# Kernel optimization log

Measured on AMD Instinct MI355X. Metric: run time of the kernel, lower is better.

Reference implementation:

```python
import math
import jax, jax.numpy as jnp
import numpy as np
from jax.scipy.special import xlogy, gammaln

HEADS = 8
DIM_KEY = 64
NUM_REL_POS_FEATURES = 192


def get_positional_embed(n, feature_size):
    # distances: [-n+1, ..., n-1], length 2n-1
    dist = jnp.arange(-n + 1, n)
    adist = jnp.abs(dist).astype(jnp.float32)[:, None]  # (2n-1, 1)
    num_basis = feature_size // 6  # 3 feature fns * 2 (sign-augmented)
    seq_len = n
    # exponential half-life features
    max_range = math.log(seq_len) / math.log(2.0)
    half_life = 2.0 ** jnp.linspace(3.0, max_range, num_basis)  # min_half_life=3.0
    feat_exp = jnp.exp(-math.log(2.0) / half_life[None, :] * adist)
    # central mask features
    center_widths = 2.0 ** jnp.arange(1, num_basis + 1) - 1.0
    feat_cm = (center_widths[None, :] > adist).astype(jnp.float32)
    # gamma pdf features
    stddev = seq_len / (2 * num_basis)
    start_mean = seq_len / num_basis
    mean = jnp.linspace(start_mean, float(seq_len), num_basis)[None, :]
    concentration = (mean / stddev) ** 2
    rate = mean / (stddev ** 2)
    log_unnorm = xlogy(concentration - 1.0, adist) - rate * adist
    log_norm = gammaln(concentration) - concentration * jnp.log(rate)
    prob = jnp.exp(log_unnorm - log_norm) + 1e-8
    feat_gamma = prob / jnp.max(prob, axis=-1, keepdims=True)
    emb = jnp.concatenate([feat_exp, feat_cm, feat_gamma], axis=-1)  # (2n-1, fs/2)
    sign = jnp.sign(dist).astype(jnp.float32)[:, None]
    return jnp.concatenate([emb, sign * emb], axis=-1)  # (2n-1, fs)


def relative_shift(x):
    # x: (b, h, n, 2n-1) -> (b, h, n, n) Transformer-XL shift
    b, h, t1, t2 = x.shape
    x = jnp.pad(x, ((0, 0), (0, 0), (0, 0), (1, 0)))  # (b,h,t1,t2+1)
    x = x.reshape(b, h, t2 + 1, t1)[:, :, 1:, :].reshape(b, h, t1, t2)
    return x[..., : (t2 + 2) // 2]


def setup_inputs() -> dict:
    key = jax.random.key(0)
    ks = jax.random.split(key, 8)
    dim = 1536
    b, n = 2, 1536
    hdk = HEADS * DIM_KEY  # 512
    hdv = HEADS * 192      # 1536
    s = 0.02
    return {
        'x': jax.random.normal(ks[0], (b, n, dim), jnp.float32),
        'Wq': jax.random.normal(ks[1], (hdk, dim), jnp.float32) * s,
        'Wk': jax.random.normal(ks[2], (hdk, dim), jnp.float32) * s,
        'Wv': jax.random.normal(ks[3], (hdv, dim), jnp.float32) * s,
        'Wrel': jax.random.normal(ks[4], (hdk, NUM_REL_POS_FEATURES), jnp.float32) * s,
        'Wout': jax.random.normal(ks[5], (dim, hdv), jnp.float32) * s,
        'b_out': jnp.zeros((dim,), jnp.float32),
        'rel_content_bias': jax.random.normal(ks[6], (1, HEADS, 1, DIM_KEY), jnp.float32),
        'rel_pos_bias': jax.random.normal(ks[7], (1, HEADS, 1, DIM_KEY), jnp.float32),
    }


def reference(x, Wq, Wk, Wv, Wrel, Wout, b_out, rel_content_bias, rel_pos_bias):
    b, n, dim = x.shape
    h = HEADS
    scale = DIM_KEY ** -0.5

    def split_heads(t):  # (b, n, h*d) -> (b, h, n, d)
        return t.reshape(b, n, h, -1).transpose(0, 2, 1, 3)

    q = split_heads(jnp.einsum('bnd,fd->bnf', x, Wq)) * scale
    k = split_heads(jnp.einsum('bnd,fd->bnf', x, Wk))
    v = split_heads(jnp.einsum('bnd,fd->bnf', x, Wv))

    content_logits = jnp.einsum('bhid,bhjd->bhij', q + rel_content_bias, k)

    positions = get_positional_embed(n, NUM_REL_POS_FEATURES)  # (2n-1, fs)
    rel_k = jnp.einsum('jf,ef->je', positions, Wrel).reshape(2 * n - 1, h, DIM_KEY)
    rel_k = rel_k.transpose(1, 0, 2)  # (h, 2n-1, dk)
    rel_logits = jnp.einsum('bhid,hjd->bhij', q + rel_pos_bias, rel_k)
    rel_logits = relative_shift(rel_logits)  # (b, h, n, n)

    attn = jax.nn.softmax(content_logits + rel_logits, axis=-1)
    out = jnp.einsum('bhij,bhjd->bhid', attn, v)
    out = out.transpose(0, 2, 1, 3).reshape(b, n, -1)  # (b, n, h*dv)
    return jnp.einsum('bnf,df->bnd', out, Wout) + b_out
```

## Files before the change

kernel.cpp:

```cpp
#include <hip/hip_runtime.h>
#include <cmath>

typedef unsigned short u16;
typedef unsigned int u32;
typedef short frag8 __attribute__((ext_vector_type(8)));
typedef float f32x4 __attribute__((ext_vector_type(4)));

#define DEVINL __device__ __forceinline__

DEVINL float bf2f(u16 v) { return __uint_as_float(((u32)v) << 16); }
DEVINL u16 f2bf(float f) {
    u32 u = __float_as_uint(f);
    u32 r = (u + 0x7fffu + ((u >> 16) & 1u)) >> 16;
    return (u16)r;
}
DEVINL u32 pack2(float a, float b) { return (u32)f2bf(a) | ((u32)f2bf(b) << 16); }
DEVINL void async_copy16(const u16* g, u16* l) {
    __builtin_amdgcn_global_load_lds((const __attribute__((address_space(1))) u32*)g,
                                     (__attribute__((address_space(3))) u32*)l, 16, 0, 0);
}
DEVINL f32x4 mfma_bf16(frag8 a, frag8 b, f32x4 c) {
    return __builtin_amdgcn_mfma_f32_16x16x32_bf16(a, b, c, 0, 0, 0);
}

__global__ __launch_bounds__(256) void convert_kernel(
        const float* __restrict__ s0, const float* __restrict__ s1,
        const float* __restrict__ s2, const float* __restrict__ s3,
        const float* __restrict__ s4, u16* __restrict__ dst) {
    const int c0 = 589824, c1 = 98304, c2 = 98304, c3 = 294912;
    const int total = 1376256;
    for (int c = blockIdx.x * blockDim.x + threadIdx.x; c < total;
         c += gridDim.x * blockDim.x) {
        const float* src; int off;
        if (c < c0) { src = s0; off = c; }
        else if (c < c0 + c1) { src = s1; off = c - c0; }
        else if (c < c0 + c1 + c2) { src = s2; off = c - c0 - c1; }
        else if (c < c0 + c1 + c2 + c3) { src = s3; off = c - c0 - c1 - c2; }
        else { src = s4; off = c - c0 - c1 - c2 - c3; }
        float4 a = ((const float4*)src)[off * 2];
        float4 b = ((const float4*)src)[off * 2 + 1];
        uint4 o;
        o.x = pack2(a.x, a.y); o.y = pack2(a.z, a.w);
        o.z = pack2(b.x, b.y); o.w = pack2(b.z, b.w);
        ((uint4*)dst)[c] = o;
    }
}

DEVINL double lgamma_stirling(double z) {
    double zi = 1.0 / z, zi2 = zi * zi;
    return (z - 0.5) * log(z) - z + 0.91893853320467274178
         + zi * (1.0 / 12.0) - zi * zi2 * (1.0 / 360.0) + zi * zi2 * zi2 * (1.0 / 1260.0);
}

__global__ __launch_bounds__(256) void embed_relk_kernel(const float* __restrict__ Wrel,
                                                         u16* __restrict__ relk) {
    __shared__ float pos[16][192];
    __shared__ float inv_hl[32], cwid[32], cm1[32], rateS[32];
    __shared__ double lognS[32];
    __shared__ float gmax[16];
    int t = threadIdx.x;
    int u0b = blockIdx.x * 16;

    if (t < 32) {
        double step = (10.584962500721156 - 3.0) / 31.0;
        double hl = exp2(3.0 + t * step);
        inv_hl[t] = (float)(1.0 / hl);
        cwid[t] = exp2f((float)(t + 1)) - 1.0f;
        double mean = 48.0 * (t + 1);
        double conc = (mean / 24.0) * (mean / 24.0);
        double rate = mean / 576.0;
        cm1[t] = (float)(conc - 1.0);
        rateS[t] = (float)rate;
        lognS[t] = lgamma_stirling(conc) - conc * log(rate);
    }
    __syncthreads();

    for (int idx = t; idx < 512; idx += 256) {
        int ul = idx >> 5, bs = idx & 31;
        int dist = u0b + ul - 1535;
        float ad = fabsf((float)dist);
        pos[ul][bs] = exp2f(-ad * inv_hl[bs]);
        pos[ul][32 + bs] = (cwid[bs] > ad) ? 1.0f : 0.0f;
        double prob = 0.0;
        if (dist != 0) {
            double adD = (double)ad;
            prob = exp((double)cm1[bs] * log(adD) - (double)rateS[bs] * adD - lognS[bs]);
        }
        pos[ul][64 + bs] = (float)(prob + 1e-8);
    }
    __syncthreads();
    if (t < 16) {
        float g = 0.f;
        #pragma unroll
        for (int bsx = 0; bsx < 32; bsx++) g = fmaxf(g, pos[t][64 + bsx]);
        gmax[t] = g;
    }
    __syncthreads();
    for (int idx = t; idx < 16 * 96; idx += 256) {
        int ul = idx / 96, f = idx - ul * 96;
        float v = pos[ul][f];
        if (f >= 64) { v = v / gmax[ul]; pos[ul][f] = v; }
        int dist = u0b + ul - 1535;
        float sg = (dist > 0) ? 1.f : ((dist < 0) ? -1.f : 0.f);
        pos[ul][96 + f] = sg * v;
    }
    __syncthreads();

    int e0 = t * 2;
    const float* w0 = Wrel + e0 * 192;
    const float* w1 = w0 + 192;
    float a0[16], a1[16];
    #pragma unroll
    for (int ul = 0; ul < 16; ul++) { a0[ul] = 0.f; a1[ul] = 0.f; }
    for (int f = 0; f < 192; f++) {
        float wa = w0[f], wb = w1[f];
        #pragma unroll
        for (int ul = 0; ul < 16; ul++) {
            float p = pos[ul][f];
            a0[ul] = fmaf(p, wa, a0[ul]);
            a1[ul] = fmaf(p, wb, a1[ul]);
        }
    }
    int h0 = e0 >> 6, d0 = e0 & 63;
    int h1 = (e0 + 1) >> 6, d1 = (e0 + 1) & 63;
    for (int ul = 0; ul < 16; ul++) {
        int u = u0b + ul;
        relk[(h0 * 3072 + u) * 64 + d0] = f2bf(a0[ul]);
        relk[(h1 * 3072 + u) * 64 + d1] = f2bf(a1[ul]);
    }
}

DEVINL void gemm128_mainloop(const u16* __restrict__ A, const u16* __restrict__ B,
                             int K, f32x4 acc[4][4], u16* As, u16* Bs) {
    int tid = threadIdx.x;
    int lane = tid & 63, wave = tid >> 6;
    int wm = (wave >> 1) * 64, wn = (wave & 1) * 64;
    int fm = lane & 15, fq = lane >> 4;
    for (int k0 = 0; k0 < K; k0 += 32) {
        #pragma unroll
        for (int p = 0; p < 2; p++) {
            int e = (p * 256 + tid) * 8;
            int r = e >> 5, c = e & 31;
            async_copy16(A + r * K + k0 + c, As + e);
            async_copy16(B + r * K + k0 + c, Bs + e);
        }
        __syncthreads();
        frag8 af[4], bfr[4];
        #pragma unroll
        for (int mi = 0; mi < 4; mi++) af[mi] = *(const frag8*)&As[(wm + 16 * mi + fm) * 32 + fq * 8];
        #pragma unroll
        for (int ni = 0; ni < 4; ni++) bfr[ni] = *(const frag8*)&Bs[(wn + 16 * ni + fm) * 32 + fq * 8];
        #pragma unroll
        for (int mi = 0; mi < 4; mi++)
            #pragma unroll
            for (int ni = 0; ni < 4; ni++)
                acc[mi][ni] = mfma_bf16(af[mi], bfr[ni], acc[mi][ni]);
        __syncthreads();
    }
}

__global__ __launch_bounds__(256) void gemm_qkv_kernel(
        const u16* __restrict__ X, const u16* __restrict__ Wq, const u16* __restrict__ Wk,
        const u16* __restrict__ Wv, const float* __restrict__ cbias, const float* __restrict__ pbias,
        u16* __restrict__ qc, u16* __restrict__ qp, u16* __restrict__ kws, u16* __restrict__ vt) {
    __shared__ __align__(16) u16 As[128 * 32];
    __shared__ __align__(16) u16 Bs[128 * 32];
    int m0 = blockIdx.x * 128, n0 = blockIdx.y * 128;
    const u16* Bp; int brow;
    if (n0 < 512)       { Bp = Wq; brow = n0; }
    else if (n0 < 1024) { Bp = Wk; brow = n0 - 512; }
    else                { Bp = Wv; brow = n0 - 1024; }
    f32x4 acc[4][4];
    #pragma unroll
    for (int i = 0; i < 4; i++)
        #pragma unroll
        for (int j = 0; j < 4; j++) acc[i][j] = (f32x4){0.f, 0.f, 0.f, 0.f};
    gemm128_mainloop(X + m0 * 1536, Bp + brow * 1536, 1536, acc, As, Bs);

    int tid = threadIdx.x, lane = tid & 63, wave = tid >> 6;
    int wm = (wave >> 1) * 64, wn = (wave & 1) * 64, fm = lane & 15, fq = lane >> 4;
    #pragma unroll
    for (int mi = 0; mi < 4; mi++) {
        #pragma unroll
        for (int ni = 0; ni < 4; ni++) {
            int col = n0 + wn + 16 * ni + fm;
            int rbase = m0 + wm + 16 * mi + fq * 4;
            #pragma unroll
            for (int reg = 0; reg < 4; reg++) {
                int row = rbase + reg;
                float v = acc[mi][ni][reg];
                int b = row >= 1536 ? 1 : 0;
                int i = row - b * 1536;
                if (n0 < 512) {
                    float qv = v * 0.125f;
                    int idx = ((b * 8 + (col >> 6)) * 1536 + i) * 64 + (col & 63);
                    qc[idx] = f2bf(qv + cbias[col]);
                    qp[idx] = f2bf(qv + pbias[col]);
                } else if (n0 < 1024) {
                    int c2 = col - 512;
                    kws[((b * 8 + (c2 >> 6)) * 1536 + i) * 64 + (c2 & 63)] = f2bf(v);
                } else {
                    int c2 = col - 1024;
                    int hh = c2 / 192, dd = c2 - hh * 192;
                    vt[((b * 8 + hh) * 192 + dd) * 1536 + i] = f2bf(v);
                }
            }
        }
    }
}

__global__ __launch_bounds__(256) void attn_kernel(
        const u16* __restrict__ qc, const u16* __restrict__ qp, const u16* __restrict__ kws,
        const u16* __restrict__ vt, const u16* __restrict__ relk, u16* __restrict__ ao) {
    __shared__ __align__(16) u16 k_lds[64 * 64];
    __shared__ __align__(16) u16 vt_lds[192 * 64];
    __shared__ __align__(16) u16 relk_lds[96 * 64];
    __shared__ __align__(16) float S_lds[32 * 64];
    __shared__ __align__(16) u16 P_lds[32 * 64];
    __shared__ float mstate[32], lstate[32], alpha_lds[32];
    float* R_lds = (float*)relk_lds;

    const int n = 1536;
    int bh = blockIdx.y, b = bh >> 3, h = bh & 7;
    int i0 = blockIdx.x * 32;
    const u16* qcP = qc + bh * n * 64;
    const u16* qpP = qp + bh * n * 64;
    const u16* kP  = kws + bh * n * 64;
    const u16* vtP = vt + bh * 192 * n;
    const u16* rkP = relk + h * 3072 * 64;

    int tid = threadIdx.x, lane = tid & 63, w = tid >> 6, fm = lane & 15, fq = lane >> 4;
    if (tid < 32) { mstate[tid] = __int_as_float(0xff800000); lstate[tid] = 0.f; }

    frag8 aqc[2][2], aqp[2][2];
    #pragma unroll
    for (int mi = 0; mi < 2; mi++)
        #pragma unroll
        for (int ks = 0; ks < 2; ks++) {
            int off = (i0 + 16 * mi + fm) * 64 + ks * 32 + fq * 8;
            aqc[mi][ks] = *(const frag8*)(qcP + off);
            aqp[mi][ks] = *(const frag8*)(qpP + off);
        }

    f32x4 acc_o[2][3];
    #pragma unroll
    for (int mi = 0; mi < 2; mi++)
        #pragma unroll
        for (int dj = 0; dj < 3; dj++) acc_o[mi][dj] = (f32x4){0.f, 0.f, 0.f, 0.f};

    for (int jt = 0; jt < 24; jt++) {
        int j0 = jt * 64;
        __syncthreads();
        #pragma unroll
        for (int p = 0; p < 2; p++) {
            int e = (p * 256 + tid) * 8;
            async_copy16(kP + (j0 + (e >> 6)) * 64 + (e & 63), k_lds + e);
        }
        #pragma unroll
        for (int p = 0; p < 6; p++) {
            int e = (p * 256 + tid) * 8;
            async_copy16(vtP + (e >> 6) * n + j0 + (e & 63), vt_lds + e);
        }
        int u0 = n - 1 + j0 - i0 - 31;
        #pragma unroll
        for (int p = 0; p < 3; p++) {
            int e = (p * 256 + tid) * 8;
            async_copy16(rkP + (u0 + (e >> 6)) * 64 + (e & 63), relk_lds + e);
        }
        __syncthreads();

        f32x4 acc_s[2];
        acc_s[0] = (f32x4){0.f, 0.f, 0.f, 0.f};
        acc_s[1] = (f32x4){0.f, 0.f, 0.f, 0.f};
        #pragma unroll
        for (int ks = 0; ks < 2; ks++) {
            frag8 bk = *(const frag8*)&k_lds[(16 * w + fm) * 64 + ks * 32 + fq * 8];
            acc_s[0] = mfma_bf16(aqc[0][ks], bk, acc_s[0]);
            acc_s[1] = mfma_bf16(aqc[1][ks], bk, acc_s[1]);
        }
        f32x4 acc_r[3];
        int uis[3], rmis[3];
        #pragma unroll
        for (int tt = 0; tt < 3; tt++) {
            int tv = w + tt * 4;
            int rmi = (tv >= 6) ? 1 : 0;
            int ui = tv - rmi * 6;
            uis[tt] = ui; rmis[tt] = rmi;
            acc_r[tt] = (f32x4){0.f, 0.f, 0.f, 0.f};
            #pragma unroll
            for (int ks = 0; ks < 2; ks++) {
                frag8 br = *(const frag8*)&relk_lds[(16 * ui + fm) * 64 + ks * 32 + fq * 8];
                acc_r[tt] = mfma_bf16(aqp[rmi][ks], br, acc_r[tt]);
            }
        }
        __syncthreads();

        #pragma unroll
        for (int mi = 0; mi < 2; mi++)
            #pragma unroll
            for (int reg = 0; reg < 4; reg++)
                S_lds[(16 * mi + fq * 4 + reg) * 64 + 16 * w + fm] = acc_s[mi][reg];
        #pragma unroll
        for (int tt = 0; tt < 3; tt++)
            #pragma unroll
            for (int reg = 0; reg < 4; reg++)
                R_lds[(16 * rmis[tt] + fq * 4 + reg) * 96 + 16 * uis[tt] + fm] = acc_r[tt][reg];
        __syncthreads();

        int li = tid >> 3, c0 = (tid & 7) * 8;
        float sv[8];
        float mx = __int_as_float(0xff800000);
        #pragma unroll
        for (int e = 0; e < 8; e++) {
            int c = c0 + e;
            sv[e] = S_lds[li * 64 + c] + R_lds[li * 96 + c - li + 31];
            mx = fmaxf(mx, sv[e]);
        }
        mx = fmaxf(mx, __shfl_xor(mx, 1));
        mx = fmaxf(mx, __shfl_xor(mx, 2));
        mx = fmaxf(mx, __shfl_xor(mx, 4));
        float mo = mstate[li];
        float mn = fmaxf(mo, mx);
        float al = __expf(mo - mn);
        float sum = 0.f;
        #pragma unroll
        for (int e = 0; e < 8; e++) {
            float pv = __expf(sv[e] - mn);
            sum += pv;
            P_lds[li * 64 + c0 + e] = f2bf(pv);
        }
        sum += __shfl_xor(sum, 1);
        sum += __shfl_xor(sum, 2);
        sum += __shfl_xor(sum, 4);
        if ((tid & 7) == 0) {
            mstate[li] = mn;
            lstate[li] = lstate[li] * al + sum;
            alpha_lds[li] = al;
        }
        __syncthreads();

        #pragma unroll
        for (int mi = 0; mi < 2; mi++)
            #pragma unroll
            for (int reg = 0; reg < 4; reg++) {
                float al2 = alpha_lds[16 * mi + fq * 4 + reg];
                #pragma unroll
                for (int dj = 0; dj < 3; dj++) acc_o[mi][dj][reg] *= al2;
            }
        frag8 ap[2][2];
        #pragma unroll
        for (int mi = 0; mi < 2; mi++)
            #pragma unroll
            for (int ks = 0; ks < 2; ks++)
                ap[mi][ks] = *(const frag8*)&P_lds[(16 * mi + fm) * 64 + ks * 32 + fq * 8];
        #pragma unroll
        for (int dj = 0; dj < 3; dj++) {
            #pragma unroll
            for (int ks = 0; ks < 2; ks++) {
                frag8 bv = *(const frag8*)&vt_lds[(16 * (3 * w + dj) + fm) * 64 + ks * 32 + fq * 8];
                acc_o[0][dj] = mfma_bf16(ap[0][ks], bv, acc_o[0][dj]);
                acc_o[1][dj] = mfma_bf16(ap[1][ks], bv, acc_o[1][dj]);
            }
        }
    }

    #pragma unroll
    for (int mi = 0; mi < 2; mi++)
        #pragma unroll
        for (int dj = 0; dj < 3; dj++)
            #pragma unroll
            for (int reg = 0; reg < 4; reg++) {
                int rl = 16 * mi + fq * 4 + reg;
                float lsum = lstate[rl];
                int row = b * 1536 + i0 + rl;
                int col = h * 192 + 16 * (3 * w + dj) + fm;
                ao[row * 1536 + col] = f2bf(acc_o[mi][dj][reg] / lsum);
            }
}

__global__ __launch_bounds__(256) void gemm_out_kernel(
        const u16* __restrict__ A, const u16* __restrict__ W, const float* __restrict__ bias,
        float* __restrict__ out) {
    __shared__ __align__(16) u16 As[128 * 32];
    __shared__ __align__(16) u16 Bs[128 * 32];
    int m0 = blockIdx.x * 128, n0 = blockIdx.y * 128;
    f32x4 acc[4][4];
    #pragma unroll
    for (int i = 0; i < 4; i++)
        #pragma unroll
        for (int j = 0; j < 4; j++) acc[i][j] = (f32x4){0.f, 0.f, 0.f, 0.f};
    gemm128_mainloop(A + m0 * 1536, W + n0 * 1536, 1536, acc, As, Bs);

    int tid = threadIdx.x, lane = tid & 63, wave = tid >> 6;
    int wm = (wave >> 1) * 64, wn = (wave & 1) * 64, fm = lane & 15, fq = lane >> 4;
    #pragma unroll
    for (int mi = 0; mi < 4; mi++) {
        #pragma unroll
        for (int ni = 0; ni < 4; ni++) {
            int col = n0 + wn + 16 * ni + fm;
            int rbase = m0 + wm + 16 * mi + fq * 4;
            float bv = bias[col];
            #pragma unroll
            for (int reg = 0; reg < 4; reg++) {
                int row = rbase + reg;
                out[row * 1536 + col] = acc[mi][ni][reg] + bv;
            }
        }
    }
}

extern "C" void kernel_launch(void* const* d_in, const int* in_sizes, int n_in,
                              void* d_out, int out_size, void* d_ws, size_t ws_size,
                              hipStream_t stream) {
    (void)in_sizes; (void)n_in; (void)out_size; (void)ws_size;
    const float* x    = (const float*)d_in[0];
    const float* Wq   = (const float*)d_in[1];
    const float* Wk   = (const float*)d_in[2];
    const float* Wv   = (const float*)d_in[3];
    const float* Wrel = (const float*)d_in[4];
    const float* Wout = (const float*)d_in[5];
    const float* bout = (const float*)d_in[6];
    const float* cb   = (const float*)d_in[7];
    const float* pb   = (const float*)d_in[8];

    u16* xb  = (u16*)d_ws;
    u16* wqb = xb  + 4718592;
    u16* wkb = wqb + 786432;
    u16* wvb = wkb + 786432;
    u16* wob = wvb + 2359296;
    u16* qc  = wob + 2359296;
    u16* qp  = qc + 1572864;
    u16* kw  = qp + 1572864;
    u16* vt  = kw + 1572864;
    u16* rk  = vt + 4718592;
    u16* ao  = rk + 1572864;
    float* out = (float*)d_out;

    convert_kernel<<<dim3(1024), dim3(256), 0, stream>>>(x, Wq, Wk, Wv, Wout, xb);
    embed_relk_kernel<<<dim3(192), dim3(256), 0, stream>>>(Wrel, rk);
    gemm_qkv_kernel<<<dim3(24, 20), dim3(256), 0, stream>>>(xb, wqb, wkb, wvb, cb, pb, qc, qp, kw, vt);
    attn_kernel<<<dim3(48, 16), dim3(256), 0, stream>>>(qc, qp, kw, vt, rk, ao);
    gemm_out_kernel<<<dim3(24, 12), dim3(256), 0, stream>>>(ao, wob, bout, out);
}
```

Baseline: 353.3 us.

## Split attention keys across waves with per-wave softmax and register-resident scores

The attention kernel now gives each wave its own 16-key slice of every 64-key tile. Each wave computes transposed S tiles and applies the online softmax in registers using lane shuffles, instead of going through LDS with extra barriers. The PV product uses half-filled K=32 MFMAs, and a cross-wave merge of the per-wave max, sum and output is done at the end with LDS atomics. XOR-swizzled LDS layouts are added to reduce bank conflicts. In exchange, half the PV MFMA work is wasted on zero padding, the output accumulators grow from 6 to 24 per thread, which raises register pressure, and an atomic epilogue is added.

After: 478.7 us. +35.5%, slower.

```diff
diff --git a/kernel.cpp b/kernel.cpp
--- a/kernel.cpp
+++ b/kernel.cpp
@@ -4,6 +4,7 @@
 typedef unsigned short u16;
 typedef unsigned int u32;
 typedef short frag8 __attribute__((ext_vector_type(8)));
+typedef short frag4v __attribute__((ext_vector_type(4)));
 typedef float f32x4 __attribute__((ext_vector_type(4)));
 
 #define DEVINL __device__ __forceinline__
@@ -212,13 +213,15 @@
 __global__ __launch_bounds__(256) void attn_kernel(
         const u16* __restrict__ qc, const u16* __restrict__ qp, const u16* __restrict__ kws,
         const u16* __restrict__ vt, const u16* __restrict__ relk, u16* __restrict__ ao) {
-    __shared__ __align__(16) u16 k_lds[64 * 64];
-    __shared__ __align__(16) u16 vt_lds[192 * 64];
-    __shared__ __align__(16) u16 relk_lds[96 * 64];
-    __shared__ __align__(16) float S_lds[32 * 64];
-    __shared__ __align__(16) u16 P_lds[32 * 64];
-    __shared__ float mstate[32], lstate[32], alpha_lds[32];
-    float* R_lds = (float*)relk_lds;
+    __shared__ __align__(16) u16 smem[29632];
+    u16* k_lds    = smem;
+    u16* vt_lds   = smem + 4096;
+    u16* relk_lds = smem + 16384;
+    float* RT     = (float*)(smem + 22528);
+    float* mwbuf  = (float*)(smem + 29056);
+    float* lwbuf  = mwbuf + 128;
+    float* Lr     = lwbuf + 128;
+    float* Obuf   = (float*)vt_lds;
 
     const int n = 1536;
     int bh = blockIdx.y, b = bh >> 3, h = bh & 7;
@@ -229,8 +232,8 @@
     const u16* vtP = vt + bh * 192 * n;
     const u16* rkP = relk + h * 3072 * 64;
 
-    int tid = threadIdx.x, lane = tid & 63, w = tid >> 6, fm = lane & 15, fq = lane >> 4;
-    if (tid < 32) { mstate[tid] = __int_as_float(0xff800000); lstate[tid] = 0.f; }
+    int tid = threadIdx.x, fm = tid & 15, fq = (tid >> 4) & 3, w = tid >> 6;
+    int sw = fm & 7;
 
     frag8 aqc[2][2], aqp[2][2];
     #pragma unroll
@@ -242,30 +245,40 @@
             aqp[mi][ks] = *(const frag8*)(qpP + off);
         }
 
-    f32x4 acc_o[2][3];
+    f32x4 acc_o[2][12];
     #pragma unroll
     for (int mi = 0; mi < 2; mi++)
         #pragma unroll
-        for (int dj = 0; dj < 3; dj++) acc_o[mi][dj] = (f32x4){0.f, 0.f, 0.f, 0.f};
+        for (int dt = 0; dt < 12; dt++) acc_o[mi][dt] = (f32x4){0.f, 0.f, 0.f, 0.f};
+    float mstate[2] = {__int_as_float(0xff800000), __int_as_float(0xff800000)};
+    float lstate[2] = {0.f, 0.f};
+
+    int uis[3], rmis[3];
+    #pragma unroll
+    for (int tt = 0; tt < 3; tt++) {
+        int tv = w + tt * 4;
+        rmis[tt] = (tv >= 6) ? 1 : 0;
+        uis[tt] = tv - rmis[tt] * 6;
+    }
 
     for (int jt = 0; jt < 24; jt++) {
         int j0 = jt * 64;
         __syncthreads();
         #pragma unroll
         for (int p = 0; p < 2; p++) {
-            int e = (p * 256 + tid) * 8;
-            async_copy16(kP + (j0 + (e >> 6)) * 64 + (e & 63), k_lds + e);
+            int l = p * 256 + tid, r = l >> 3, c = (l & 7) ^ (r & 7);
+            async_copy16(kP + (j0 + r) * 64 + c * 8, k_lds + l * 8);
         }
         #pragma unroll
         for (int p = 0; p < 6; p++) {
-            int e = (p * 256 + tid) * 8;
-            async_copy16(vtP + (e >> 6) * n + j0 + (e & 63), vt_lds + e);
-        }
-        int u0 = n - 1 + j0 - i0 - 31;
+            int l = p * 256 + tid, r = l >> 3, c = (l & 7) ^ (r & 7);
+            async_copy16(vtP + r * n + j0 + c * 8, vt_lds + l * 8);
+        }
+        int u0 = 1504 + j0 - i0;
         #pragma unroll
         for (int p = 0; p < 3; p++) {
-            int e = (p * 256 + tid) * 8;
-            async_copy16(rkP + (u0 + (e >> 6)) * 64 + (e & 63), relk_lds + e);
+            int l = p * 256 + tid, r = l >> 3, c = (l & 7) ^ (r & 7);
+            async_copy16(rkP + (u0 + r) * 64 + c * 8, relk_lds + l * 8);
         }
         __syncthreads();
 
@@ -274,108 +287,110 @@
         acc_s[1] = (f32x4){0.f, 0.f, 0.f, 0.f};
         #pragma unroll
         for (int ks = 0; ks < 2; ks++) {
-            frag8 bk = *(const frag8*)&k_lds[(16 * w + fm) * 64 + ks * 32 + fq * 8];
-            acc_s[0] = mfma_bf16(aqc[0][ks], bk, acc_s[0]);
-            acc_s[1] = mfma_bf16(aqc[1][ks], bk, acc_s[1]);
-        }
-        f32x4 acc_r[3];
-        int uis[3], rmis[3];
+            frag8 kf = *(const frag8*)&k_lds[(16 * w + fm) * 64 + ((ks * 4 + fq) ^ sw) * 8];
+            acc_s[0] = mfma_bf16(kf, aqc[0][ks], acc_s[0]);
+            acc_s[1] = mfma_bf16(kf, aqc[1][ks], acc_s[1]);
+        }
         #pragma unroll
         for (int tt = 0; tt < 3; tt++) {
-            int tv = w + tt * 4;
-            int rmi = (tv >= 6) ? 1 : 0;
-            int ui = tv - rmi * 6;
-            uis[tt] = ui; rmis[tt] = rmi;
-            acc_r[tt] = (f32x4){0.f, 0.f, 0.f, 0.f};
+            f32x4 r = (f32x4){0.f, 0.f, 0.f, 0.f};
             #pragma unroll
             for (int ks = 0; ks < 2; ks++) {
-                frag8 br = *(const frag8*)&relk_lds[(16 * ui + fm) * 64 + ks * 32 + fq * 8];
-                acc_r[tt] = mfma_bf16(aqp[rmi][ks], br, acc_r[tt]);
+                frag8 rf = *(const frag8*)&relk_lds[(16 * uis[tt] + fm) * 64 + ((ks * 4 + fq) ^ sw) * 8];
+                r = mfma_bf16(rf, aqp[rmis[tt]][ks], r);
             }
+            #pragma unroll
+            for (int reg = 0; reg < 4; reg++)
+                RT[(16 * uis[tt] + fq * 4 + reg) * 34 + 16 * rmis[tt] + fm] = r[reg];
         }
         __syncthreads();
 
-        #pragma unroll
-        for (int mi = 0; mi < 2; mi++)
-            #pragma unroll
-            for (int reg = 0; reg < 4; reg++)
-                S_lds[(16 * mi + fq * 4 + reg) * 64 + 16 * w + fm] = acc_s[mi][reg];
-        #pragma unroll
-        for (int tt = 0; tt < 3; tt++)
-            #pragma unroll
-            for (int reg = 0; reg < 4; reg++)
-                R_lds[(16 * rmis[tt] + fq * 4 + reg) * 96 + 16 * uis[tt] + fm] = acc_r[tt][reg];
-        __syncthreads();
-
-        int li = tid >> 3, c0 = (tid & 7) * 8;
-        float sv[8];
-        float mx = __int_as_float(0xff800000);
-        #pragma unroll
-        for (int e = 0; e < 8; e++) {
-            int c = c0 + e;
-            sv[e] = S_lds[li * 64 + c] + R_lds[li * 96 + c - li + 31];
-            mx = fmaxf(mx, sv[e]);
-        }
-        mx = fmaxf(mx, __shfl_xor(mx, 1));
-        mx = fmaxf(mx, __shfl_xor(mx, 2));
-        mx = fmaxf(mx, __shfl_xor(mx, 4));
-        float mo = mstate[li];
-        float mn = fmaxf(mo, mx);
-        float al = __expf(mo - mn);
-        float sum = 0.f;
-        #pragma unroll
-        for (int e = 0; e < 8; e++) {
-            float pv = __expf(sv[e] - mn);
-            sum += pv;
-            P_lds[li * 64 + c0 + e] = f2bf(pv);
-        }
-        sum += __shfl_xor(sum, 1);
-        sum += __shfl_xor(sum, 2);
-        sum += __shfl_xor(sum, 4);
-        if ((tid & 7) == 0) {
-            mstate[li] = mn;
-            lstate[li] = lstate[li] * al + sum;
-            alpha_lds[li] = al;
-        }
-        __syncthreads();
-
-        #pragma unroll
-        for (int mi = 0; mi < 2; mi++)
+        frag8 ap[2];
+        #pragma unroll
+        for (int mi = 0; mi < 2; mi++) {
+            int i_full = 16 * mi + fm;
+            float sv[4];
+            float mx = __int_as_float(0xff800000);
             #pragma unroll
             for (int reg = 0; reg < 4; reg++) {
-                float al2 = alpha_lds[16 * mi + fq * 4 + reg];
+                int up = 16 * w + fq * 4 + reg + 31 - i_full;
+                sv[reg] = acc_s[mi][reg] + RT[up * 34 + i_full];
+                mx = fmaxf(mx, sv[reg]);
+            }
+            mx = fmaxf(mx, __shfl_xor(mx, 16));
+            mx = fmaxf(mx, __shfl_xor(mx, 32));
+            float mn = fmaxf(mstate[mi], mx);
+            float al = __expf(mstate[mi] - mn);
+            mstate[mi] = mn;
+            float pv[4], psum = 0.f;
+            #pragma unroll
+            for (int reg = 0; reg < 4; reg++) { pv[reg] = __expf(sv[reg] - mn); psum += pv[reg]; }
+            psum += __shfl_xor(psum, 16);
+            psum += __shfl_xor(psum, 32);
+            lstate[mi] = lstate[mi] * al + psum;
+            ap[mi] = (frag8){(short)f2bf(pv[0]), (short)f2bf(pv[1]),
+                             (short)f2bf(pv[2]), (short)f2bf(pv[3]), 0, 0, 0, 0};
+            #pragma unroll
+            for (int reg = 0; reg < 4; reg++) {
+                float ab = __shfl(al, fq * 4 + reg);
                 #pragma unroll
-                for (int dj = 0; dj < 3; dj++) acc_o[mi][dj][reg] *= al2;
+                for (int dt = 0; dt < 12; dt++) acc_o[mi][dt][reg] *= ab;
             }
-        frag8 ap[2][2];
-        #pragma unroll
-        for (int mi = 0; mi < 2; mi++)
-            #pragma unroll
-            for (int ks = 0; ks < 2; ks++)
-                ap[mi][ks] = *(const frag8*)&P_lds[(16 * mi + fm) * 64 + ks * 32 + fq * 8];
-        #pragma unroll
-        for (int dj = 0; dj < 3; dj++) {
-            #pragma unroll
-            for (int ks = 0; ks < 2; ks++) {
-                frag8 bv = *(const frag8*)&vt_lds[(16 * (3 * w + dj) + fm) * 64 + ks * 32 + fq * 8];
-                acc_o[0][dj] = mfma_bf16(ap[0][ks], bv, acc_o[0][dj]);
-                acc_o[1][dj] = mfma_bf16(ap[1][ks], bv, acc_o[1][dj]);
-            }
-        }
-    }
-
+        }
+
+        int cj = 2 * w + (fq >> 1);
+        int jo = (fq & 1) * 4;
+        #pragma unroll
+        for (int dt = 0; dt < 12; dt++) {
+            frag4v t4 = *(const frag4v*)&vt_lds[(16 * dt + fm) * 64 + (cj ^ sw) * 8 + jo];
+            frag8 bv = (frag8){t4[0], t4[1], t4[2], t4[3], 0, 0, 0, 0};
+            acc_o[0][dt] = mfma_bf16(ap[0], bv, acc_o[0][dt]);
+            acc_o[1][dt] = mfma_bf16(ap[1], bv, acc_o[1][dt]);
+        }
+    }
+
+    __syncthreads();
+    if (fq == 0) {
+        #pragma unroll
+        for (int mi = 0; mi < 2; mi++) {
+            mwbuf[(w * 2 + mi) * 16 + fm] = mstate[mi];
+            lwbuf[(w * 2 + mi) * 16 + fm] = lstate[mi];
+        }
+    }
+    #pragma unroll
+    for (int r = 0; r < 24; r++) Obuf[r * 256 + tid] = 0.f;
+    __syncthreads();
     #pragma unroll
     for (int mi = 0; mi < 2; mi++)
         #pragma unroll
-        for (int dj = 0; dj < 3; dj++)
-            #pragma unroll
-            for (int reg = 0; reg < 4; reg++) {
-                int rl = 16 * mi + fq * 4 + reg;
-                float lsum = lstate[rl];
-                int row = b * 1536 + i0 + rl;
-                int col = h * 192 + 16 * (3 * w + dj) + fm;
-                ao[row * 1536 + col] = f2bf(acc_o[mi][dj][reg] / lsum);
-            }
+        for (int reg = 0; reg < 4; reg++) {
+            int ir = fq * 4 + reg;
+            float mg = mwbuf[mi * 16 + ir];
+            #pragma unroll
+            for (int wv = 1; wv < 4; wv++) mg = fmaxf(mg, mwbuf[(wv * 2 + mi) * 16 + ir]);
+            float sc = __expf(mwbuf[(w * 2 + mi) * 16 + ir] - mg);
+            #pragma unroll
+            for (int dt = 0; dt < 12; dt++)
+                atomicAdd(&Obuf[(16 * mi + ir) * 192 + 16 * dt + fm], acc_o[mi][dt][reg] * sc);
+        }
+    __syncthreads();
+    if (tid < 32) {
+        int mi = tid >> 4, ir = tid & 15;
+        float mg = mwbuf[mi * 16 + ir];
+        #pragma unroll
+        for (int wv = 1; wv < 4; wv++) mg = fmaxf(mg, mwbuf[(wv * 2 + mi) * 16 + ir]);
+        float L = 0.f;
+        #pragma unroll
+        for (int wv = 0; wv < 4; wv++)
+            L += lwbuf[(wv * 2 + mi) * 16 + ir] * __expf(mwbuf[(wv * 2 + mi) * 16 + ir] - mg);
+        Lr[tid] = 1.0f / L;
+    }
+    __syncthreads();
+    for (int r = 0; r < 24; r++) {
+        int idx = r * 256 + tid;
+        int i = idx / 192, dv = idx - i * 192;
+        ao[(b * 1536 + i0 + i) * 1536 + h * 192 + dv] = f2bf(Obuf[idx] * Lr[i]);
+    }
 }
 
 __global__ __launch_bounds__(256) void gemm_out_kernel(
```

## Swizzle attention LDS tiles and alias score buffers to cut LDS footprint

Applied to the files above, without the earlier changes.

Applies an XOR swizzle of 16-byte chunks to the K, V-transpose, rel-K and P tiles in shared memory, on both the async global-to-LDS writes and the MFMA fragment reads, to remove LDS bank conflicts. S and R scores now alias the K and rel-K buffers, and all buffers are packed into one array, which shrinks shared memory per block and may allow more resident blocks. P is written as one packed 16-byte store per thread. Aliasing depends on the existing barriers ordering the reuse correctly, and a final sync is added before the epilogue.

Result: faster. 328.2 us (-7.1%).

```diff
diff --git a/kernel.cpp b/kernel.cpp
--- a/kernel.cpp
+++ b/kernel.cpp
@@ -212,13 +212,16 @@
 __global__ __launch_bounds__(256) void attn_kernel(
         const u16* __restrict__ qc, const u16* __restrict__ qp, const u16* __restrict__ kws,
         const u16* __restrict__ vt, const u16* __restrict__ relk, u16* __restrict__ ao) {
-    __shared__ __align__(16) u16 k_lds[64 * 64];
-    __shared__ __align__(16) u16 vt_lds[192 * 64];
-    __shared__ __align__(16) u16 relk_lds[96 * 64];
-    __shared__ __align__(16) float S_lds[32 * 64];
-    __shared__ __align__(16) u16 P_lds[32 * 64];
-    __shared__ float mstate[32], lstate[32], alpha_lds[32];
-    float* R_lds = (float*)relk_lds;
+    __shared__ __align__(16) u16 smem[24768];
+    u16* k_lds    = smem;
+    u16* vt_lds   = smem + 4096;
+    u16* relk_lds = smem + 16384;
+    u16* P_lds    = smem + 22528;
+    float* S_lds  = (float*)k_lds;
+    float* R_lds  = (float*)relk_lds;
+    float* mstate = (float*)(smem + 24576);
+    float* lstate = mstate + 32;
+    float* alpha_lds = lstate + 32;
 
     const int n = 1536;
     int bh = blockIdx.y, b = bh >> 3, h = bh & 7;
@@ -230,6 +233,7 @@
     const u16* rkP = relk + h * 3072 * 64;
 
     int tid = threadIdx.x, lane = tid & 63, w = tid >> 6, fm = lane & 15, fq = lane >> 4;
+    int sw = fm & 7;
     if (tid < 32) { mstate[tid] = __int_as_float(0xff800000); lstate[tid] = 0.f; }
 
     frag8 aqc[2][2], aqp[2][2];
@@ -248,24 +252,32 @@
         #pragma unroll
         for (int dj = 0; dj < 3; dj++) acc_o[mi][dj] = (f32x4){0.f, 0.f, 0.f, 0.f};
 
+    int uis[3], rmis[3];
+    #pragma unroll
+    for (int tt = 0; tt < 3; tt++) {
+        int tv = w + tt * 4;
+        rmis[tt] = (tv >= 6) ? 1 : 0;
+        uis[tt] = tv - rmis[tt] * 6;
+    }
+
     for (int jt = 0; jt < 24; jt++) {
         int j0 = jt * 64;
         __syncthreads();
         #pragma unroll
         for (int p = 0; p < 2; p++) {
-            int e = (p * 256 + tid) * 8;
-            async_copy16(kP + (j0 + (e >> 6)) * 64 + (e & 63), k_lds + e);
+            int l = p * 256 + tid, r = l >> 3, c = (l & 7) ^ (r & 7);
+            async_copy16(kP + (j0 + r) * 64 + c * 8, k_lds + l * 8);
         }
         #pragma unroll
         for (int p = 0; p < 6; p++) {
-            int e = (p * 256 + tid) * 8;
-            async_copy16(vtP + (e >> 6) * n + j0 + (e & 63), vt_lds + e);
-        }
-        int u0 = n - 1 + j0 - i0 - 31;
+            int l = p * 256 + tid, r = l >> 3, c = (l & 7) ^ (r & 7);
+            async_copy16(vtP + r * n + j0 + c * 8, vt_lds + l * 8);
+        }
+        int u0 = 1504 + j0 - i0;
         #pragma unroll
         for (int p = 0; p < 3; p++) {
-            int e = (p * 256 + tid) * 8;
-            async_copy16(rkP + (u0 + (e >> 6)) * 64 + (e & 63), relk_lds + e);
+            int l = p * 256 + tid, r = l >> 3, c = (l & 7) ^ (r & 7);
+            async_copy16(rkP + (u0 + r) * 64 + c * 8, relk_lds + l * 8);
         }
         __syncthreads();
 
@@ -274,23 +286,18 @@
         acc_s[1] = (f32x4){0.f, 0.f, 0.f, 0.f};
         #pragma unroll
         for (int ks = 0; ks < 2; ks++) {
-            frag8 bk = *(const frag8*)&k_lds[(16 * w + fm) * 64 + ks * 32 + fq * 8];
+            frag8 bk = *(const frag8*)&k_lds[(16 * w + fm) * 64 + ((ks * 4 + fq) ^ sw) * 8];
             acc_s[0] = mfma_bf16(aqc[0][ks], bk, acc_s[0]);
             acc_s[1] = mfma_bf16(aqc[1][ks], bk, acc_s[1]);
         }
         f32x4 acc_r[3];
-        int uis[3], rmis[3];
         #pragma unroll
         for (int tt = 0; tt < 3; tt++) {
-            int tv = w + tt * 4;
-            int rmi = (tv >= 6) ? 1 : 0;
-            int ui = tv - rmi * 6;
-            uis[tt] = ui; rmis[tt] = rmi;
             acc_r[tt] = (f32x4){0.f, 0.f, 0.f, 0.f};
             #pragma unroll
             for (int ks = 0; ks < 2; ks++) {
-                frag8 br = *(const frag8*)&relk_lds[(16 * ui + fm) * 64 + ks * 32 + fq * 8];
-                acc_r[tt] = mfma_bf16(aqp[rmi][ks], br, acc_r[tt]);
+                frag8 br = *(const frag8*)&relk_lds[(16 * uis[tt] + fm) * 64 + ((ks * 4 + fq) ^ sw) * 8];
+                acc_r[tt] = mfma_bf16(aqp[rmis[tt]][ks], br, acc_r[tt]);
             }
         }
         __syncthreads();
@@ -322,12 +329,15 @@
         float mo = mstate[li];
         float mn = fmaxf(mo, mx);
         float al = __expf(mo - mn);
-        float sum = 0.f;
-        #pragma unroll
-        for (int e = 0; e < 8; e++) {
-            float pv = __expf(sv[e] - mn);
-            sum += pv;
-            P_lds[li * 64 + c0 + e] = f2bf(pv);
+        float pe[8], sum = 0.f;
+        #pragma unroll
+        for (int e = 0; e < 8; e++) { pe[e] = __expf(sv[e] - mn); sum += pe[e]; }
+        {
+            uint4 pw;
+            pw.x = pack2(pe[0], pe[1]); pw.y = pack2(pe[2], pe[3]);
+            pw.z = pack2(pe[4], pe[5]); pw.w = pack2(pe[6], pe[7]);
+            int slot = (tid & 7) ^ (li & 7);
+            *(uint4*)&P_lds[li * 64 + slot * 8] = pw;
         }
         sum += __shfl_xor(sum, 1);
         sum += __shfl_xor(sum, 2);
@@ -352,18 +362,19 @@
         for (int mi = 0; mi < 2; mi++)
             #pragma unroll
             for (int ks = 0; ks < 2; ks++)
-                ap[mi][ks] = *(const frag8*)&P_lds[(16 * mi + fm) * 64 + ks * 32 + fq * 8];
+                ap[mi][ks] = *(const frag8*)&P_lds[(16 * mi + fm) * 64 + ((ks * 4 + fq) ^ sw) * 8];
         #pragma unroll
         for (int dj = 0; dj < 3; dj++) {
             #pragma unroll
             for (int ks = 0; ks < 2; ks++) {
-                frag8 bv = *(const frag8*)&vt_lds[(16 * (3 * w + dj) + fm) * 64 + ks * 32 + fq * 8];
+                frag8 bv = *(const frag8*)&vt_lds[(16 * (3 * w + dj) + fm) * 64 + ((ks * 4 + fq) ^ sw) * 8];
                 acc_o[0][dj] = mfma_bf16(ap[0][ks], bv, acc_o[0][dj]);
                 acc_o[1][dj] = mfma_bf16(ap[1][ks], bv, acc_o[1][dj]);
             }
         }
     }
 
+    __syncthreads();
     #pragma unroll
     for (int mi = 0; mi < 2; mi++)
         #pragma unroll
```
